# Performance work log

Measured on AMD Instinct MI355X. Metric: run time of the kernel, lower is better.

Reference implementation:

```python
import jax, jax.numpy as jnp
import numpy as np

N_USERS = 100000
N_ITEMS = 40000
N_NODES = N_USERS + N_ITEMS
D = 64
IMG_DIM = 2048
TXT_DIM = 384
N_EDGES = 1000000
N_LAYERS = 2
ALPHA = 0.2


def setup_inputs() -> dict:
    key = jax.random.key(0)
    ks = jax.random.split(key, 10)
    edge_index = jax.random.randint(ks[0], (2, N_EDGES), 0, N_NODES, dtype=jnp.int64 if jax.config.jax_enable_x64 else jnp.int32)
    edge_weight = jax.random.uniform(ks[1], (N_EDGES, 1), dtype=jnp.float32)
    image_feats = jax.random.normal(ks[2], (N_ITEMS, IMG_DIM), dtype=jnp.float32)
    text_feats = jax.random.normal(ks[3], (N_ITEMS, TXT_DIM), dtype=jnp.float32)
    s_img = 1.0 / np.sqrt(IMG_DIM)
    s_txt = 1.0 / np.sqrt(TXT_DIM)
    image_trs_w = jax.random.uniform(ks[4], (IMG_DIM, D), jnp.float32, -s_img, s_img)
    image_trs_b = jnp.zeros((D,), jnp.float32)
    text_trs_w = jax.random.uniform(ks[5], (TXT_DIM, D), jnp.float32, -s_txt, s_txt)
    text_trs_b = jnp.zeros((D,), jnp.float32)
    image_pref = jax.random.normal(ks[6], (N_USERS, D), jnp.float32) * 0.1
    text_pref = jax.random.normal(ks[7], (N_USERS, D), jnp.float32) * 0.1
    return {
        "edge_index": edge_index,
        "edge_weight": edge_weight,
        "image_feats": image_feats,
        "text_feats": text_feats,
        "image_trs_w": image_trs_w,
        "image_trs_b": image_trs_b,
        "text_trs_w": text_trs_w,
        "text_trs_b": text_trs_b,
        "image_pref": image_pref,
        "text_pref": text_pref,
    }


def _l2_normalize(x):
    # matches F.normalize(x, p=2, dim=1, eps=1e-12)
    n = jnp.linalg.norm(x, axis=1, keepdims=True)
    return x / jnp.maximum(n, 1e-12)


def _propagate(x, src, dst, w):
    # PyG 'add' aggregation: message = x[src] * w, scatter-add into dst
    msgs = x[src] * w  # [E, D]
    return jax.ops.segment_sum(msgs, dst, num_segments=N_NODES)


def reference(edge_index, edge_weight, image_feats, text_feats,
              image_trs_w, image_trs_b, text_trs_w, text_trs_b,
              image_pref, text_pref):
    src, dst = edge_index[0], edge_index[1]

    image_emb = _l2_normalize(image_feats @ image_trs_w + image_trs_b)
    text_emb = _l2_normalize(text_feats @ text_trs_w + text_trs_b)

    ego_img = jnp.concatenate([image_pref, image_emb], axis=0)  # [N, D]
    ego_txt = jnp.concatenate([text_pref, text_emb], axis=0)    # [N, D]

    for _ in range(N_LAYERS):
        ego_img = _propagate(ego_img, src, dst, edge_weight) + ALPHA * ego_img
        ego_txt = _propagate(ego_txt, src, dst, edge_weight) + ALPHA * ego_txt

    # stack final modality embeddings; rows 0:N_USERS are user preferences,
    # N_USERS: are item embeddings (torch.split boundary)
    return jnp.stack([ego_img, ego_txt], axis=0)  # [2, N, D]
```

## Files before the change

### kernel.cpp

```cpp
#include <hip/hip_runtime.h>

#define N_USERS 100000
#define N_ITEMS 40000
#define NN      140000
#define N_EDGES 1000000
#define ALPHA   0.2f

typedef short bf16x8 __attribute__((ext_vector_type(8)));
typedef float f32x4  __attribute__((ext_vector_type(4)));

__device__ __forceinline__ unsigned short f2b(float x) {
    unsigned u = __builtin_bit_cast(unsigned, x);
    unsigned r = (u + 0x7FFFu + ((u >> 16) & 1u)) >> 16;
    return (unsigned short)r;
}
__device__ __forceinline__ unsigned cvtpk(float lo, float hi) {
    unsigned r;
    asm("v_cvt_pk_bf16_f32 %0, %1, %2" : "=v"(r) : "v"(lo), "v"(hi));
    return r;
}
__device__ __forceinline__ float blo(unsigned u) { return __builtin_bit_cast(float, u << 16); }
__device__ __forceinline__ float bhi(unsigned u) { return __builtin_bit_cast(float, u & 0xFFFF0000u); }

__device__ __forceinline__ void gl_lds16(const void* g, void* l) {
    __builtin_amdgcn_global_load_lds(
        (const __attribute__((address_space(1))) void*)g,
        (__attribute__((address_space(3))) void*)l, 16, 0, 0);
}

#define PREP_CP   6250
#define PREP_CI   (PREP_CP + 512)
#define PREP_CT   (PREP_CI + 96)
#define PREP_ALL  (PREP_CT + 3907)

__device__ __forceinline__ int wt_pos(int k, int n) {
    return ((k >> 5) * 4 + (n >> 4)) * 512 + ((((k >> 3) & 3) * 16) + (n & 15)) * 8 + (k & 7);
}

__global__ __launch_bounds__(256)
void prep(const float* __restrict__ imgp, const float* __restrict__ txtp,
          unsigned short* __restrict__ X,
          const float* __restrict__ Wi, short* __restrict__ WtImg,
          const float* __restrict__ Wx, short* __restrict__ WtTxt,
          const int* __restrict__ ei, int* __restrict__ deg,
          int* __restrict__ rank)
{
    int b = blockIdx.x, t = threadIdx.x;
    if (b < PREP_CP) {
        int tid = b * 256 + t;
        if (tid >= N_USERS * 16) return;
        int i  = tid >> 4;
        int c8 = tid & 15;
        const float* src = (c8 < 8) ? &imgp[(size_t)i * 64 + c8 * 8]
                                    : &txtp[(size_t)i * 64 + (c8 - 8) * 8];
        float4 a = *reinterpret_cast<const float4*>(src);
        float4 c = *reinterpret_cast<const float4*>(src + 4);
        int4 o = make_int4((int)cvtpk(a.x, a.y), (int)cvtpk(a.z, a.w),
                           (int)cvtpk(c.x, c.y), (int)cvtpk(c.z, c.w));
        *reinterpret_cast<int4*>(&X[(size_t)i * 128 + c8 * 8]) = o;
    } else if (b < PREP_CI) {
        int tid = (b - PREP_CP) * 256 + t;
        int k = tid >> 6, n = tid & 63;
        WtImg[wt_pos(k, n)] = (short)f2b(Wi[tid]);
    } else if (b < PREP_CT) {
        int tid = (b - PREP_CI) * 256 + t;
        if (tid >= 384 * 64) return;
        int k = tid >> 6, n = tid & 63;
        WtTxt[wt_pos(k, n)] = (short)f2b(Wx[tid]);
    } else {
        int e = (b - PREP_CT) * 256 + t;
        if (e < N_EDGES) {
            int d = ei[N_EDGES + e];
            int r = atomicAdd(&deg[d], 1);
            rank[e] = r;
        }
    }
}

template<int K, int COLOFF>
__device__ __forceinline__
void gemm_body(int bx, const float* __restrict__ A, const short* __restrict__ Wt,
               const float* __restrict__ bias, unsigned short* __restrict__ X,
               float* ldsA, short* ldsB)
{
    constexpr int NT = K / 64;
    const int t    = threadIdx.x;
    const int wid  = t >> 6;
    const int lane = t & 63;
    const int lo   = lane & 15;
    const int g    = lane >> 4;
    const int r0   = bx * 64;

    f32x4 acc[4];
    #pragma unroll
    for (int ct = 0; ct < 4; ++ct) acc[ct] = (f32x4){0.f, 0.f, 0.f, 0.f};

    auto stage = [&](int buf, int kt) {
        int k0 = kt * 64;
        #pragma unroll
        for (int i = 0; i < 4; ++i) {
            int c     = i * 4 + wid;
            int row_t = c * 4 + g;
            int u_log = lo ^ (row_t & 15);
            const float* gp = A + (size_t)(r0 + row_t) * K + k0 + u_log * 4;
            gl_lds16(gp, ldsA + buf * 4096 + c * 256);
        }
        #pragma unroll
        for (int i2 = 0; i2 < 2; ++i2) {
            int c2 = i2 * 4 + wid;
            const short* gp = Wt + ((size_t)kt * 8 + c2) * 512 + lane * 8;
            gl_lds16(gp, ldsB + buf * 4096 + c2 * 512);
        }
    };

    auto compute = [&](int buf) {
        int row_t = wid * 16 + lo;
        const float* baseA = ldsA + buf * 4096 + row_t * 64;
        const short* baseB = ldsB + buf * 4096;
        #pragma unroll
        for (int m = 0; m < 2; ++m) {
            int u0 = (m * 8 + 2 * g) ^ lo;
            int u1 = (m * 8 + 2 * g + 1) ^ lo;
            float4 xa = *reinterpret_cast<const float4*>(baseA + u0 * 4);
            float4 ya = *reinterpret_cast<const float4*>(baseA + u1 * 4);
            int4 ai = make_int4((int)cvtpk(xa.x, xa.y), (int)cvtpk(xa.z, xa.w),
                                (int)cvtpk(ya.x, ya.y), (int)cvtpk(ya.z, ya.w));
            bf16x8 a = __builtin_bit_cast(bf16x8, ai);
            #pragma unroll
            for (int ct = 0; ct < 4; ++ct) {
                int4 w = *reinterpret_cast<const int4*>(baseB + (m * 4 + ct) * 512 + lane * 8);
                bf16x8 bb = __builtin_bit_cast(bf16x8, w);
                acc[ct] = __builtin_amdgcn_mfma_f32_16x16x32_bf16(a, bb, acc[ct], 0, 0, 0);
            }
        }
    };

    stage(0, 0);
    for (int kt = 0; kt < NT; ++kt) {
        if (kt + 1 < NT) {
            stage((kt + 1) & 1, kt + 1);
            asm volatile("s_waitcnt vmcnt(6)" ::: "memory");
        } else {
            asm volatile("s_waitcnt vmcnt(0)" ::: "memory");
        }
        __builtin_amdgcn_s_barrier();
        __builtin_amdgcn_sched_barrier(0);
        compute(kt & 1);
        __builtin_amdgcn_s_barrier();
    }

    float bia[4];
    #pragma unroll
    for (int ct = 0; ct < 4; ++ct) bia[ct] = bias[ct * 16 + lo];

    int r0w = r0 + wid * 16;
    #pragma unroll
    for (int r = 0; r < 4; ++r) {
        float v[4];
        float ss = 0.f;
        #pragma unroll
        for (int ct = 0; ct < 4; ++ct) { v[ct] = acc[ct][r] + bia[ct]; ss += v[ct] * v[ct]; }
        ss += __shfl_xor(ss, 1);
        ss += __shfl_xor(ss, 2);
        ss += __shfl_xor(ss, 4);
        ss += __shfl_xor(ss, 8);
        float sc = 1.0f / fmaxf(sqrtf(ss), 1e-12f);
        int grow = r0w + g * 4 + r;
        unsigned short* dst = &X[(size_t)(N_USERS + grow) * 128 + COLOFF + lo];
        #pragma unroll
        for (int ct = 0; ct < 4; ++ct) dst[ct * 16] = f2b(v[ct] * sc);
    }
}

__global__ __launch_bounds__(256)
void gemm_fill(const float* __restrict__ Ai, const short* __restrict__ WtImg,
               const float* __restrict__ bi,
               const float* __restrict__ Ax, const short* __restrict__ WtTxt,
               const float* __restrict__ bx, unsigned short* __restrict__ X,
               const int* __restrict__ ei, const float* __restrict__ ew,
               const int* __restrict__ row_ptr, const int* __restrict__ rank,
               int2* __restrict__ epk)
{
    __shared__ float ldsA[8192];
    __shared__ __align__(16) short ldsB[8192];
    int b = blockIdx.x;
    if (b < 625)       gemm_body<2048, 0 >(b, Ai, WtImg, bi, X, ldsA, ldsB);
    else if (b < 1250) gemm_body< 384, 64>(b - 625, Ax, WtTxt, bx, X, ldsA, ldsB);
    else {
        int e = (b - 1250) * 256 + threadIdx.x;
        if (e >= N_EDGES) return;
        int s = ei[e];
        int d = ei[N_EDGES + e];
        int p = row_ptr[d] + rank[e];
        epk[p] = make_int2(s, __builtin_bit_cast(int, ew[e]));
    }
}

__global__ void scan1(const int* __restrict__ deg, int* __restrict__ row_ptr,
                      int* __restrict__ blockSums)
{
    __shared__ int ts[256];
    int t = threadIdx.x, b = blockIdx.x;
    int base = b * 1024 + t * 4;
    int v[4]; int s = 0;
    #pragma unroll
    for (int j = 0; j < 4; j++) {
        v[j] = (base + j < NN) ? deg[base + j] : 0;
        s += v[j];
    }
    ts[t] = s;
    __syncthreads();
    for (int off = 1; off < 256; off <<= 1) {
        int x = (t >= off) ? ts[t - off] : 0;
        __syncthreads();
        ts[t] += x;
        __syncthreads();
    }
    int excl = ts[t] - s;
    int run = excl;
    #pragma unroll
    for (int j = 0; j < 4; j++) {
        if (base + j < NN) row_ptr[base + j] = run;
        run += v[j];
    }
    if (t == 255) blockSums[b] = ts[255];
}

__global__ void scan23(const int* __restrict__ blockSums, int* __restrict__ row_ptr)
{
    __shared__ int ts[256];
    int t = threadIdx.x, b = blockIdx.x;
    ts[t] = (t < b) ? blockSums[t] : 0;
    __syncthreads();
    for (int off = 128; off > 0; off >>= 1) {
        if (t < off) ts[t] += ts[t + off];
        __syncthreads();
    }
    int off0 = ts[0];
    int base = b * 1024 + t * 4;
    #pragma unroll
    for (int j = 0; j < 4; j++) {
        int idx = base + j;
        if (idx < NN) row_ptr[idx] += off0;
    }
    if (b == 0 && t == 0) row_ptr[NN] = N_EDGES;
}

template<bool FINAL>
__global__ __launch_bounds__(256)
void propagate(const unsigned short* __restrict__ Xin, const int* __restrict__ row_ptr,
               const int2* __restrict__ epk, void* __restrict__ outv)
{
    int lane = threadIdx.x & 63;
    int gl   = lane & 15;
    int gb   = lane & 48;
    int node = blockIdx.x * 16 + (threadIdx.x >> 4);
    int e0 = row_ptr[node];
    int e1 = row_ptr[node + 1];
    float a0 = 0.f, a1 = 0.f, a2 = 0.f, a3 = 0.f;
    float a4 = 0.f, a5 = 0.f, a6 = 0.f, a7 = 0.f;

    for (int base = e0; base < e1; base += 16) {
        int cnt = e1 - base; if (cnt > 16) cnt = 16;
        int sv = 0, wvb = 0;
        if (base + gl < e1) {
            int2 ev = epk[base + gl];
            sv = ev.x; wvb = ev.y;
        }
        float wv = __builtin_bit_cast(float, wvb);
        int i = 0;
        for (; i + 1 < cnt; i += 2) {
            int   s0 = __shfl(sv, gb + i);
            int   s1 = __shfl(sv, gb + i + 1);
            float w0 = __shfl(wv, gb + i);
            float w1 = __shfl(wv, gb + i + 1);
            uint4 u0 = *reinterpret_cast<const uint4*>(&Xin[(size_t)s0 * 128 + gl * 8]);
            uint4 u1 = *reinterpret_cast<const uint4*>(&Xin[(size_t)s1 * 128 + gl * 8]);
            a0 = fmaf(w0, blo(u0.x), a0); a1 = fmaf(w0, bhi(u0.x), a1);
            a2 = fmaf(w0, blo(u0.y), a2); a3 = fmaf(w0, bhi(u0.y), a3);
            a4 = fmaf(w0, blo(u0.z), a4); a5 = fmaf(w0, bhi(u0.z), a5);
            a6 = fmaf(w0, blo(u0.w), a6); a7 = fmaf(w0, bhi(u0.w), a7);
            a0 = fmaf(w1, blo(u1.x), a0); a1 = fmaf(w1, bhi(u1.x), a1);
            a2 = fmaf(w1, blo(u1.y), a2); a3 = fmaf(w1, bhi(u1.y), a3);
            a4 = fmaf(w1, blo(u1.z), a4); a5 = fmaf(w1, bhi(u1.z), a5);
            a6 = fmaf(w1, blo(u1.w), a6); a7 = fmaf(w1, bhi(u1.w), a7);
        }
        if (i < cnt) {
            int   s0 = __shfl(sv, gb + i);
            float w0 = __shfl(wv, gb + i);
            uint4 u0 = *reinterpret_cast<const uint4*>(&Xin[(size_t)s0 * 128 + gl * 8]);
            a0 = fmaf(w0, blo(u0.x), a0); a1 = fmaf(w0, bhi(u0.x), a1);
            a2 = fmaf(w0, blo(u0.y), a2); a3 = fmaf(w0, bhi(u0.y), a3);
            a4 = fmaf(w0, blo(u0.z), a4); a5 = fmaf(w0, bhi(u0.z), a5);
            a6 = fmaf(w0, blo(u0.w), a6); a7 = fmaf(w0, bhi(u0.w), a7);
        }
    }

    uint4 us = *reinterpret_cast<const uint4*>(&Xin[(size_t)node * 128 + gl * 8]);
    a0 += ALPHA * blo(us.x); a1 += ALPHA * bhi(us.x);
    a2 += ALPHA * blo(us.y); a3 += ALPHA * bhi(us.y);
    a4 += ALPHA * blo(us.z); a5 += ALPHA * bhi(us.z);
    a6 += ALPHA * blo(us.w); a7 += ALPHA * bhi(us.w);

    if (!FINAL) {
        unsigned short* out = (unsigned short*)outv;
        uint4 p;
        p.x = cvtpk(a0, a1); p.y = cvtpk(a2, a3);
        p.z = cvtpk(a4, a5); p.w = cvtpk(a6, a7);
        *reinterpret_cast<uint4*>(&out[(size_t)node * 128 + gl * 8]) = p;
    } else {
        float* out = (float*)outv;
        int d = gl * 8;
        float* dst = (d < 64) ? &out[(size_t)node * 64 + d]
                              : &out[(size_t)NN * 64 + (size_t)node * 64 + (d - 64)];
        *reinterpret_cast<float4*>(dst)     = make_float4(a0, a1, a2, a3);
        *reinterpret_cast<float4*>(dst + 4) = make_float4(a4, a5, a6, a7);
    }
}

extern "C" void kernel_launch(void* const* d_in, const int* in_sizes, int n_in,
                              void* d_out, int out_size, void* d_ws, size_t ws_size,
                              hipStream_t stream)
{
    const int*   ei       = (const int*)d_in[0];
    const float* ew       = (const float*)d_in[1];
    const float* img_feat = (const float*)d_in[2];
    const float* txt_feat = (const float*)d_in[3];
    const float* img_w    = (const float*)d_in[4];
    const float* img_b    = (const float*)d_in[5];
    const float* txt_w    = (const float*)d_in[6];
    const float* txt_b    = (const float*)d_in[7];
    const float* img_pref = (const float*)d_in[8];
    const float* txt_pref = (const float*)d_in[9];
    float* out = (float*)d_out;

    const size_t XBYTES = (size_t)NN * 128 * 2;
    char* ws = (char*)d_ws;
    size_t off = 0;
    auto alloc = [&](size_t bytes) -> void* {
        void* p = ws + off;
        off = (off + bytes + 255) & ~(size_t)255;
        return p;
    };
    unsigned short* Xa = (unsigned short*)alloc(XBYTES);
    unsigned short* Xb = (unsigned short*)alloc(XBYTES);
    int*   deg     = (int*)alloc((size_t)NN * 4);
    int*   row_ptr = (int*)alloc((size_t)(NN + 1) * 4);
    int*   rank    = (int*)alloc((size_t)N_EDGES * 4);
    int2*  epk     = (int2*)alloc((size_t)N_EDGES * 8);
    int*   bsums   = (int*)alloc(256 * 4);
    short* WtImg   = (short*)alloc((size_t)2048 * 64 * 2);
    short* WtTxt   = (short*)alloc((size_t)384 * 64 * 2);

    hipMemsetAsync(deg, 0, (size_t)NN * 4, stream);

    prep<<<PREP_ALL, 256, 0, stream>>>(img_pref, txt_pref, Xa,
                                       img_w, WtImg, txt_w, WtTxt, ei, deg, rank);

    scan1<<<137, 256, 0, stream>>>(deg, row_ptr, bsums);
    scan23<<<137, 256, 0, stream>>>(bsums, row_ptr);

    gemm_fill<<<1250 + 3907, 256, 0, stream>>>(img_feat, WtImg, img_b,
                                               txt_feat, WtTxt, txt_b, Xa,
                                               ei, ew, row_ptr, rank, epk);

    propagate<false><<<8750, 256, 0, stream>>>(Xa, row_ptr, epk, Xb);
    propagate<true ><<<8750, 256, 0, stream>>>(Xb, row_ptr, epk, out);
}
```

Baseline: 294.4 us.

## Fuse all stages into one cooperative persistent kernel with grid syncs

Replaces the memset and six separate kernel launches with a single cooperative persistent kernel. Each former kernel becomes a grid-stride loop over work units, and the stages are separated by grid.sync barriers. This removes launch gaps and the memset, at the cost of grid-wide barrier overhead. It also caps occupancy at launch_bounds(256,3) with a shared LDS union, which may hurt the latency-bound propagate phases that previously ran at higher occupancy.

```diff
diff --git a/kernel.cpp b/kernel.cpp
--- a/kernel.cpp
+++ b/kernel.cpp
@@ -1,4 +1,7 @@
 #include <hip/hip_runtime.h>
+#include <hip/hip_cooperative_groups.h>
+
+namespace cg = cooperative_groups;
 
 #define N_USERS 100000
 #define N_ITEMS 40000
@@ -32,41 +35,43 @@
 #define PREP_CI   (PREP_CP + 512)
 #define PREP_CT   (PREP_CI + 96)
 #define PREP_ALL  (PREP_CT + 3907)
+#define NU_GEMMFILL (1250 + 3907)
+#define NU_PROP     8750
 
 __device__ __forceinline__ int wt_pos(int k, int n) {
     return ((k >> 5) * 4 + (n >> 4)) * 512 + ((((k >> 3) & 3) * 16) + (n & 15)) * 8 + (k & 7);
 }
 
-__global__ __launch_bounds__(256)
-void prep(const float* __restrict__ imgp, const float* __restrict__ txtp,
-          unsigned short* __restrict__ X,
-          const float* __restrict__ Wi, short* __restrict__ WtImg,
-          const float* __restrict__ Wx, short* __restrict__ WtTxt,
-          const int* __restrict__ ei, int* __restrict__ deg,
-          int* __restrict__ rank)
-{
-    int b = blockIdx.x, t = threadIdx.x;
+__device__ __forceinline__
+void prep_unit(int b, int t, const float* __restrict__ imgp, const float* __restrict__ txtp,
+               unsigned short* __restrict__ X,
+               const float* __restrict__ Wi, short* __restrict__ WtImg,
+               const float* __restrict__ Wx, short* __restrict__ WtTxt,
+               const int* __restrict__ ei, int* __restrict__ deg, int* __restrict__ rank)
+{
     if (b < PREP_CP) {
         int tid = b * 256 + t;
-        if (tid >= N_USERS * 16) return;
-        int i  = tid >> 4;
-        int c8 = tid & 15;
-        const float* src = (c8 < 8) ? &imgp[(size_t)i * 64 + c8 * 8]
-                                    : &txtp[(size_t)i * 64 + (c8 - 8) * 8];
-        float4 a = *reinterpret_cast<const float4*>(src);
-        float4 c = *reinterpret_cast<const float4*>(src + 4);
-        int4 o = make_int4((int)cvtpk(a.x, a.y), (int)cvtpk(a.z, a.w),
-                           (int)cvtpk(c.x, c.y), (int)cvtpk(c.z, c.w));
-        *reinterpret_cast<int4*>(&X[(size_t)i * 128 + c8 * 8]) = o;
+        if (tid < N_USERS * 16) {
+            int i  = tid >> 4;
+            int c8 = tid & 15;
+            const float* src = (c8 < 8) ? &imgp[(size_t)i * 64 + c8 * 8]
+                                        : &txtp[(size_t)i * 64 + (c8 - 8) * 8];
+            float4 a = *reinterpret_cast<const float4*>(src);
+            float4 c = *reinterpret_cast<const float4*>(src + 4);
+            int4 o = make_int4((int)cvtpk(a.x, a.y), (int)cvtpk(a.z, a.w),
+                               (int)cvtpk(c.x, c.y), (int)cvtpk(c.z, c.w));
+            *reinterpret_cast<int4*>(&X[(size_t)i * 128 + c8 * 8]) = o;
+        }
     } else if (b < PREP_CI) {
         int tid = (b - PREP_CP) * 256 + t;
         int k = tid >> 6, n = tid & 63;
         WtImg[wt_pos(k, n)] = (short)f2b(Wi[tid]);
     } else if (b < PREP_CT) {
         int tid = (b - PREP_CI) * 256 + t;
-        if (tid >= 384 * 64) return;
-        int k = tid >> 6, n = tid & 63;
-        WtTxt[wt_pos(k, n)] = (short)f2b(Wx[tid]);
+        if (tid < 384 * 64) {
+            int k = tid >> 6, n = tid & 63;
+            WtTxt[wt_pos(k, n)] = (short)f2b(Wx[tid]);
+        }
     } else {
         int e = (b - PREP_CT) * 256 + t;
         if (e < N_EDGES) {
@@ -75,6 +80,57 @@
             rank[e] = r;
         }
     }
+}
+
+__device__ __forceinline__
+void scan1_unit(int b, int t, int* ts, const int* __restrict__ deg,
+                int* __restrict__ row_ptr, int* __restrict__ blockSums)
+{
+    int base = b * 1024 + t * 4;
+    int v[4]; int s = 0;
+    #pragma unroll
+    for (int j = 0; j < 4; j++) {
+        v[j] = (base + j < NN) ? deg[base + j] : 0;
+        s += v[j];
+    }
+    ts[t] = s;
+    __syncthreads();
+    for (int off = 1; off < 256; off <<= 1) {
+        int x = (t >= off) ? ts[t - off] : 0;
+        __syncthreads();
+        ts[t] += x;
+        __syncthreads();
+    }
+    int excl = ts[t] - s;
+    int run = excl;
+    #pragma unroll
+    for (int j = 0; j < 4; j++) {
+        if (base + j < NN) row_ptr[base + j] = run;
+        run += v[j];
+    }
+    if (t == 255) blockSums[b] = ts[255];
+    __syncthreads();
+}
+
+__device__ __forceinline__
+void scan23_unit(int b, int t, int* ts, const int* __restrict__ blockSums,
+                 int* __restrict__ row_ptr)
+{
+    ts[t] = (t < b) ? blockSums[t] : 0;
+    __syncthreads();
+    for (int off = 128; off > 0; off >>= 1) {
+        if (t < off) ts[t] += ts[t + off];
+        __syncthreads();
+    }
+    int off0 = ts[0];
+    int base = b * 1024 + t * 4;
+    #pragma unroll
+    for (int j = 0; j < 4; j++) {
+        int idx = base + j;
+        if (idx < NN) row_ptr[idx] += off0;
+    }
+    if (b == 0 && t == 0) row_ptr[NN] = N_EDGES;
+    __syncthreads();
 }
 
 template<int K, int COLOFF>
@@ -172,89 +228,16 @@
     }
 }
 
-__global__ __launch_bounds__(256)
-void gemm_fill(const float* __restrict__ Ai, const short* __restrict__ WtImg,
-               const float* __restrict__ bi,
-               const float* __restrict__ Ax, const short* __restrict__ WtTxt,
-               const float* __restrict__ bx, unsigned short* __restrict__ X,
-               const int* __restrict__ ei, const float* __restrict__ ew,
-               const int* __restrict__ row_ptr, const int* __restrict__ rank,
-               int2* __restrict__ epk)
-{
-    __shared__ float ldsA[8192];
-    __shared__ __align__(16) short ldsB[8192];
-    int b = blockIdx.x;
-    if (b < 625)       gemm_body<2048, 0 >(b, Ai, WtImg, bi, X, ldsA, ldsB);
-    else if (b < 1250) gemm_body< 384, 64>(b - 625, Ax, WtTxt, bx, X, ldsA, ldsB);
-    else {
-        int e = (b - 1250) * 256 + threadIdx.x;
-        if (e >= N_EDGES) return;
-        int s = ei[e];
-        int d = ei[N_EDGES + e];
-        int p = row_ptr[d] + rank[e];
-        epk[p] = make_int2(s, __builtin_bit_cast(int, ew[e]));
-    }
-}
-
-__global__ void scan1(const int* __restrict__ deg, int* __restrict__ row_ptr,
-                      int* __restrict__ blockSums)
-{
-    __shared__ int ts[256];
-    int t = threadIdx.x, b = blockIdx.x;
-    int base = b * 1024 + t * 4;
-    int v[4]; int s = 0;
-    #pragma unroll
-    for (int j = 0; j < 4; j++) {
-        v[j] = (base + j < NN) ? deg[base + j] : 0;
-        s += v[j];
-    }
-    ts[t] = s;
-    __syncthreads();
-    for (int off = 1; off < 256; off <<= 1) {
-        int x = (t >= off) ? ts[t - off] : 0;
-        __syncthreads();
-        ts[t] += x;
-        __syncthreads();
-    }
-    int excl = ts[t] - s;
-    int run = excl;
-    #pragma unroll
-    for (int j = 0; j < 4; j++) {
-        if (base + j < NN) row_ptr[base + j] = run;
-        run += v[j];
-    }
-    if (t == 255) blockSums[b] = ts[255];
-}
-
-__global__ void scan23(const int* __restrict__ blockSums, int* __restrict__ row_ptr)
-{
-    __shared__ int ts[256];
-    int t = threadIdx.x, b = blockIdx.x;
-    ts[t] = (t < b) ? blockSums[t] : 0;
-    __syncthreads();
-    for (int off = 128; off > 0; off >>= 1) {
-        if (t < off) ts[t] += ts[t + off];
-        __syncthreads();
-    }
-    int off0 = ts[0];
-    int base = b * 1024 + t * 4;
-    #pragma unroll
-    for (int j = 0; j < 4; j++) {
-        int idx = base + j;
-        if (idx < NN) row_ptr[idx] += off0;
-    }
-    if (b == 0 && t == 0) row_ptr[NN] = N_EDGES;
-}
-
 template<bool FINAL>
-__global__ __launch_bounds__(256)
-void propagate(const unsigned short* __restrict__ Xin, const int* __restrict__ row_ptr,
-               const int2* __restrict__ epk, void* __restrict__ outv)
-{
-    int lane = threadIdx.x & 63;
+__device__ __forceinline__
+void prop_unit(int u, int t, const unsigned short* __restrict__ Xin,
+               const int* __restrict__ row_ptr, const int2* __restrict__ epk,
+               void* __restrict__ outv)
+{
+    int lane = t & 63;
     int gl   = lane & 15;
     int gb   = lane & 48;
-    int node = blockIdx.x * 16 + (threadIdx.x >> 4);
+    int node = u * 16 + (t >> 4);
     int e0 = row_ptr[node];
     int e1 = row_ptr[node + 1];
     float a0 = 0.f, a1 = 0.f, a2 = 0.f, a3 = 0.f;
@@ -318,6 +301,70 @@
     }
 }
 
+__global__ __launch_bounds__(256, 3)
+void mega(const int* __restrict__ ei, const float* __restrict__ ew,
+          const float* __restrict__ Ai, const float* __restrict__ Ax,
+          const float* __restrict__ Wi, const float* __restrict__ bi,
+          const float* __restrict__ Wx, const float* __restrict__ bx,
+          const float* __restrict__ imgp, const float* __restrict__ txtp,
+          float* __restrict__ out,
+          unsigned short* __restrict__ Xa, unsigned short* __restrict__ Xb,
+          int* __restrict__ deg, int* __restrict__ row_ptr,
+          int* __restrict__ rank, int2* __restrict__ epk,
+          int* __restrict__ bsums,
+          short* __restrict__ WtImg, short* __restrict__ WtTxt)
+{
+    __shared__ union {
+        struct { float A[8192]; __align__(16) short B[8192]; } g;
+        int ts[256];
+    } sh;
+
+    cg::grid_group grid = cg::this_grid();
+    const int bid = blockIdx.x, t = threadIdx.x, nb = gridDim.x;
+
+    for (int i = bid * 256 + t; i < NN; i += nb * 256) deg[i] = 0;
+    __threadfence();
+    grid.sync();
+
+    for (int u = bid; u < PREP_ALL; u += nb)
+        prep_unit(u, t, imgp, txtp, Xa, Wi, WtImg, Wx, WtTxt, ei, deg, rank);
+    __threadfence();
+    grid.sync();
+
+    for (int u = bid; u < 137; u += nb)
+        scan1_unit(u, t, sh.ts, deg, row_ptr, bsums);
+    __threadfence();
+    grid.sync();
+
+    for (int u = bid; u < 137; u += nb)
+        scan23_unit(u, t, sh.ts, bsums, row_ptr);
+    __threadfence();
+    grid.sync();
+
+    for (int u = bid; u < NU_GEMMFILL; u += nb) {
+        if (u < 625)       gemm_body<2048, 0 >(u, Ai, WtImg, bi, Xa, sh.g.A, sh.g.B);
+        else if (u < 1250) gemm_body< 384, 64>(u - 625, Ax, WtTxt, bx, Xa, sh.g.A, sh.g.B);
+        else {
+            int e = (u - 1250) * 256 + t;
+            if (e < N_EDGES) {
+                int s = ei[e];
+                int d = ei[N_EDGES + e];
+                epk[row_ptr[d] + rank[e]] = make_int2(s, __builtin_bit_cast(int, ew[e]));
+            }
+        }
+    }
+    __threadfence();
+    grid.sync();
+
+    for (int u = bid; u < NU_PROP; u += nb)
+        prop_unit<false>(u, t, Xa, row_ptr, epk, Xb);
+    __threadfence();
+    grid.sync();
+
+    for (int u = bid; u < NU_PROP; u += nb)
+        prop_unit<true>(u, t, Xb, row_ptr, epk, out);
+}
+
 extern "C" void kernel_launch(void* const* d_in, const int* in_sizes, int n_in,
                               void* d_out, int out_size, void* d_ws, size_t ws_size,
                               hipStream_t stream)
@@ -352,18 +399,19 @@
     short* WtImg   = (short*)alloc((size_t)2048 * 64 * 2);
     short* WtTxt   = (short*)alloc((size_t)384 * 64 * 2);
 
-    hipMemsetAsync(deg, 0, (size_t)NN * 4, stream);
-
-    prep<<<PREP_ALL, 256, 0, stream>>>(img_pref, txt_pref, Xa,
-                                       img_w, WtImg, txt_w, WtTxt, ei, deg, rank);
-
-    scan1<<<137, 256, 0, stream>>>(deg, row_ptr, bsums);
-    scan23<<<137, 256, 0, stream>>>(bsums, row_ptr);
-
-    gemm_fill<<<1250 + 3907, 256, 0, stream>>>(img_feat, WtImg, img_b,
-                                               txt_feat, WtTxt, txt_b, Xa,
-                                               ei, ew, row_ptr, rank, epk);
-
-    propagate<false><<<8750, 256, 0, stream>>>(Xa, row_ptr, epk, Xb);
-    propagate<true ><<<8750, 256, 0, stream>>>(Xb, row_ptr, epk, out);
-}
+    int maxb = 0;
+    hipOccupancyMaxActiveBlocksPerMultiprocessor(&maxb, mega, 256, 0);
+    if (maxb < 1) maxb = 1;
+    int nb = maxb * 256;
+    if (nb > 2048) nb = 2048;
+
+    void* args[] = {
+        (void*)&ei, (void*)&ew, (void*)&img_feat, (void*)&txt_feat,
+        (void*)&img_w, (void*)&img_b, (void*)&txt_w, (void*)&txt_b,
+        (void*)&img_pref, (void*)&txt_pref, (void*)&out,
+        (void*)&Xa, (void*)&Xb, (void*)&deg, (void*)&row_ptr,
+        (void*)&rank, (void*)&epk, (void*)&bsums, (void*)&WtImg, (void*)&WtTxt
+    };
+    hipLaunchCooperativeKernel((const void*)mega, dim3(nb), dim3(256),
+                               args, 0, stream);
+}
```

After: 744.0 us. +152.7%, slower.

## Split image GEMM along K into four chunks with a separate reduce-normalize pass

Applied to the files above, without the earlier changes.

The image projection (K=2048) is split into four K-chunks of 512, so the GEMM launches 2500 blocks instead of 625. Each block writes fp32 partial sums to a workspace buffer, and a new reduce_norm kernel sums the partials, adds the bias, L2-normalizes and writes bf16 into X. The goal is to fix the load imbalance where long-K blocks dominate the tail. In exchange it adds about 41 MB of partial-sum write and read traffic plus one more kernel launch. A fallback keeps the original fused path when the workspace is too small.

```diff
diff --git a/kernel.cpp b/kernel.cpp
--- a/kernel.cpp
+++ b/kernel.cpp
@@ -77,38 +77,40 @@
     }
 }
 
-template<int K, int COLOFF>
+template<int K, int KCH, int COLOFF, bool SPLIT>
 __device__ __forceinline__
-void gemm_body(int bx, const float* __restrict__ A, const short* __restrict__ Wt,
+void gemm_body(int rb, int c, const float* __restrict__ A, const short* __restrict__ Wt,
                const float* __restrict__ bias, unsigned short* __restrict__ X,
-               float* ldsA, short* ldsB)
-{
-    constexpr int NT = K / 64;
+               float* __restrict__ P, float* ldsA, short* ldsB)
+{
+    constexpr int NT = KCH / 64;
     const int t    = threadIdx.x;
     const int wid  = t >> 6;
     const int lane = t & 63;
     const int lo   = lane & 15;
     const int g    = lane >> 4;
-    const int r0   = bx * 64;
+    const int r0   = rb * 64;
+    const int kb   = c * KCH;
+    const int tb   = c * NT;
 
     f32x4 acc[4];
     #pragma unroll
     for (int ct = 0; ct < 4; ++ct) acc[ct] = (f32x4){0.f, 0.f, 0.f, 0.f};
 
     auto stage = [&](int buf, int kt) {
-        int k0 = kt * 64;
+        int k0 = kb + kt * 64;
         #pragma unroll
         for (int i = 0; i < 4; ++i) {
-            int c     = i * 4 + wid;
-            int row_t = c * 4 + g;
+            int cc    = i * 4 + wid;
+            int row_t = cc * 4 + g;
             int u_log = lo ^ (row_t & 15);
             const float* gp = A + (size_t)(r0 + row_t) * K + k0 + u_log * 4;
-            gl_lds16(gp, ldsA + buf * 4096 + c * 256);
+            gl_lds16(gp, ldsA + buf * 4096 + cc * 256);
         }
         #pragma unroll
         for (int i2 = 0; i2 < 2; ++i2) {
             int c2 = i2 * 4 + wid;
-            const short* gp = Wt + ((size_t)kt * 8 + c2) * 512 + lane * 8;
+            const short* gp = Wt + ((size_t)(tb + kt) * 8 + c2) * 512 + lane * 8;
             gl_lds16(gp, ldsB + buf * 4096 + c2 * 512);
         }
     };
@@ -149,43 +151,79 @@
         __builtin_amdgcn_s_barrier();
     }
 
-    float bia[4];
-    #pragma unroll
-    for (int ct = 0; ct < 4; ++ct) bia[ct] = bias[ct * 16 + lo];
-
     int r0w = r0 + wid * 16;
-    #pragma unroll
-    for (int r = 0; r < 4; ++r) {
-        float v[4];
-        float ss = 0.f;
-        #pragma unroll
-        for (int ct = 0; ct < 4; ++ct) { v[ct] = acc[ct][r] + bia[ct]; ss += v[ct] * v[ct]; }
-        ss += __shfl_xor(ss, 1);
-        ss += __shfl_xor(ss, 2);
-        ss += __shfl_xor(ss, 4);
-        ss += __shfl_xor(ss, 8);
-        float sc = 1.0f / fmaxf(sqrtf(ss), 1e-12f);
-        int grow = r0w + g * 4 + r;
-        unsigned short* dst = &X[(size_t)(N_USERS + grow) * 128 + COLOFF + lo];
-        #pragma unroll
-        for (int ct = 0; ct < 4; ++ct) dst[ct * 16] = f2b(v[ct] * sc);
+    if (SPLIT) {
+        #pragma unroll
+        for (int r = 0; r < 4; ++r) {
+            int grow = r0w + g * 4 + r;
+            float* dst = P + ((size_t)c * 40000 + grow) * 64 + lo;
+            #pragma unroll
+            for (int ct = 0; ct < 4; ++ct) dst[ct * 16] = acc[ct][r];
+        }
+    } else {
+        float bia[4];
+        #pragma unroll
+        for (int ct = 0; ct < 4; ++ct) bia[ct] = bias[ct * 16 + lo];
+        #pragma unroll
+        for (int r = 0; r < 4; ++r) {
+            float v[4];
+            float ss = 0.f;
+            #pragma unroll
+            for (int ct = 0; ct < 4; ++ct) { v[ct] = acc[ct][r] + bia[ct]; ss += v[ct] * v[ct]; }
+            ss += __shfl_xor(ss, 1);
+            ss += __shfl_xor(ss, 2);
+            ss += __shfl_xor(ss, 4);
+            ss += __shfl_xor(ss, 8);
+            float sc = 1.0f / fmaxf(sqrtf(ss), 1e-12f);
+            int grow = r0w + g * 4 + r;
+            unsigned short* dst = &X[(size_t)(N_USERS + grow) * 128 + COLOFF + lo];
+            #pragma unroll
+            for (int ct = 0; ct < 4; ++ct) dst[ct * 16] = f2b(v[ct] * sc);
+        }
     }
 }
 
 __global__ __launch_bounds__(256)
-void gemm_fill(const float* __restrict__ Ai, const short* __restrict__ WtImg,
-               const float* __restrict__ bi,
-               const float* __restrict__ Ax, const short* __restrict__ WtTxt,
-               const float* __restrict__ bx, unsigned short* __restrict__ X,
-               const int* __restrict__ ei, const float* __restrict__ ew,
-               const int* __restrict__ row_ptr, const int* __restrict__ rank,
-               int2* __restrict__ epk)
+void gemm_fill_split(const float* __restrict__ Ai, const short* __restrict__ WtImg,
+                     const float* __restrict__ bi,
+                     const float* __restrict__ Ax, const short* __restrict__ WtTxt,
+                     const float* __restrict__ bx, unsigned short* __restrict__ X,
+                     float* __restrict__ P,
+                     const int* __restrict__ ei, const float* __restrict__ ew,
+                     const int* __restrict__ row_ptr, const int* __restrict__ rank,
+                     int2* __restrict__ epk)
 {
     __shared__ float ldsA[8192];
     __shared__ __align__(16) short ldsB[8192];
     int b = blockIdx.x;
-    if (b < 625)       gemm_body<2048, 0 >(b, Ai, WtImg, bi, X, ldsA, ldsB);
-    else if (b < 1250) gemm_body< 384, 64>(b - 625, Ax, WtTxt, bx, X, ldsA, ldsB);
+    if (b < 2500) {
+        gemm_body<2048, 512, 0, true>(b >> 2, b & 3, Ai, WtImg, bi, X, P, ldsA, ldsB);
+    } else if (b < 3125) {
+        gemm_body<384, 384, 64, false>(b - 2500, 0, Ax, WtTxt, bx, X, P, ldsA, ldsB);
+    } else {
+        int e = (b - 3125) * 256 + threadIdx.x;
+        if (e >= N_EDGES) return;
+        int s = ei[e];
+        int d = ei[N_EDGES + e];
+        int p = row_ptr[d] + rank[e];
+        epk[p] = make_int2(s, __builtin_bit_cast(int, ew[e]));
+    }
+}
+
+__global__ __launch_bounds__(256)
+void gemm_fill_flat(const float* __restrict__ Ai, const short* __restrict__ WtImg,
+                    const float* __restrict__ bi,
+                    const float* __restrict__ Ax, const short* __restrict__ WtTxt,
+                    const float* __restrict__ bx, unsigned short* __restrict__ X,
+                    const int* __restrict__ ei, const float* __restrict__ ew,
+                    const int* __restrict__ row_ptr, const int* __restrict__ rank,
+                    int2* __restrict__ epk)
+{
+    __shared__ float ldsA[8192];
+    __shared__ __align__(16) short ldsB[8192];
+    int b = blockIdx.x;
+    if (b < 625)       gemm_body<2048, 2048, 0, false>(b, 0, Ai, WtImg, bi, X, nullptr, ldsA, ldsB);
+    else if (b < 1250) gemm_body< 384,  384, 64, false>(b - 625, 0, Ax, WtTxt, bx, X, nullptr, ldsA, ldsB);
     else {
         int e = (b - 1250) * 256 + threadIdx.x;
         if (e >= N_EDGES) return;
@@ -194,6 +232,28 @@
         int p = row_ptr[d] + rank[e];
         epk[p] = make_int2(s, __builtin_bit_cast(int, ew[e]));
     }
+}
+
+__global__ __launch_bounds__(256)
+void reduce_norm(const float* __restrict__ P, const float* __restrict__ bias,
+                 unsigned short* __restrict__ X)
+{
+    int lane = threadIdx.x & 63;
+    int row  = blockIdx.x * 4 + (threadIdx.x >> 6);
+    float v = P[(size_t)row * 64 + lane]
+            + P[((size_t)40000  + row) * 64 + lane]
+            + P[((size_t)80000  + row) * 64 + lane]
+            + P[((size_t)120000 + row) * 64 + lane]
+            + bias[lane];
+    float ss = v * v;
+    ss += __shfl_xor(ss, 1);
+    ss += __shfl_xor(ss, 2);
+    ss += __shfl_xor(ss, 4);
+    ss += __shfl_xor(ss, 8);
+    ss += __shfl_xor(ss, 16);
+    ss += __shfl_xor(ss, 32);
+    float sc = 1.0f / fmaxf(sqrtf(ss), 1e-12f);
+    X[(size_t)(N_USERS + row) * 128 + lane] = f2b(v * sc);
 }
 
 __global__ void scan1(const int* __restrict__ deg, int* __restrict__ row_ptr,
@@ -335,6 +395,7 @@
     float* out = (float*)d_out;
 
     const size_t XBYTES = (size_t)NN * 128 * 2;
+    const size_t PBYTES = (size_t)4 * 40000 * 64 * 4;
     char* ws = (char*)d_ws;
     size_t off = 0;
     auto alloc = [&](size_t bytes) -> void* {
@@ -351,6 +412,8 @@
     int*   bsums   = (int*)alloc(256 * 4);
     short* WtImg   = (short*)alloc((size_t)2048 * 64 * 2);
     short* WtTxt   = (short*)alloc((size_t)384 * 64 * 2);
+    bool haveP = (off + PBYTES) <= ws_size;
+    float* P = haveP ? (float*)alloc(PBYTES) : nullptr;
 
     hipMemsetAsync(deg, 0, (size_t)NN * 4, stream);
 
@@ -360,9 +423,16 @@
     scan1<<<137, 256, 0, stream>>>(deg, row_ptr, bsums);
     scan23<<<137, 256, 0, stream>>>(bsums, row_ptr);
 
-    gemm_fill<<<1250 + 3907, 256, 0, stream>>>(img_feat, WtImg, img_b,
-                                               txt_feat, WtTxt, txt_b, Xa,
-                                               ei, ew, row_ptr, rank, epk);
+    if (haveP) {
+        gemm_fill_split<<<3125 + 3907, 256, 0, stream>>>(
+            img_feat, WtImg, img_b, txt_feat, WtTxt, txt_b, Xa, P,
+            ei, ew, row_ptr, rank, epk);
+        reduce_norm<<<10000, 256, 0, stream>>>(P, img_b, Xa);
+    } else {
+        gemm_fill_flat<<<1250 + 3907, 256, 0, stream>>>(
+            img_feat, WtImg, img_b, txt_feat, WtTxt, txt_b, Xa,
+            ei, ew, row_ptr, rank, epk);
+    }
 
     propagate<false><<<8750, 256, 0, stream>>>(Xa, row_ptr, epk, Xb);
     propagate<true ><<<8750, 256, 0, stream>>>(Xb, row_ptr, epk, out);
```

New measurement: 293.4 us (median of 2 runs). About the same (-0.3%).
